# Performance work log

Measured on AMD Instinct MI355X. Metric: run time of the kernel, lower is better.

Reference implementation:

```python
import jax, jax.numpy as jnp
import numpy as np

EPS_GN = 1e-8
EPS_ATTN = 1e-8


def setup_inputs() -> dict:
    key = jax.random.key(0)
    ks = jax.random.split(key, 13)
    B, C, N = 4, 512, 2048
    s = 0.02
    return {
        "x": jax.random.normal(ks[0], (B, C, N), jnp.float32),
        "dw_w": jax.random.normal(ks[1], (C, 3), jnp.float32) * s,
        "pw_w": jax.random.normal(ks[2], (C, C), jnp.float32) * s,
        "u_w": jax.random.normal(ks[3], (2 * C, C), jnp.float32) * s,
        "u_b": jax.random.normal(ks[4], (2 * C,), jnp.float32) * s,
        "v_w": jax.random.normal(ks[5], (2 * C, C), jnp.float32) * s,
        "v_b": jax.random.normal(ks[6], (2 * C,), jnp.float32) * s,
        "h_w": jax.random.normal(ks[7], (C, C), jnp.float32) * s,
        "h_b": jax.random.normal(ks[8], (C,), jnp.float32) * s,
        "q_w": jax.random.normal(ks[9], (C, C), jnp.float32) * s,
        "k_w": jax.random.normal(ks[10], (C, C), jnp.float32) * s,
        "o_w": jax.random.normal(ks[11], (C, 2 * C), jnp.float32) * s,
        "o_b": jax.random.normal(ks[12], (C,), jnp.float32) * s,
    }


def reference(x, dw_w, pw_w, u_w, u_b, v_w, v_b, h_w, h_b, q_w, k_w, o_w, o_b):
    # x: [B, C, N]
    C = x.shape[1]
    # GroupNorm(1, C): normalize over (C, N) per sample; affine is identity-init
    # in torch but we follow the module math with default weight=1, bias=0
    mean = jnp.mean(x, axis=(1, 2), keepdims=True)
    var = jnp.var(x, axis=(1, 2), keepdims=True)
    z = (x - mean) * jax.lax.rsqrt(var + EPS_GN)

    # local depthwise conv k=3, pad=1 (cross-correlation), no bias
    zp = jnp.pad(z, ((0, 0), (0, 0), (1, 1)))
    dw = (dw_w[:, 0, None] * zp[:, :, :-2]
          + dw_w[:, 1, None] * zp[:, :, 1:-1]
          + dw_w[:, 2, None] * zp[:, :, 2:])
    # pointwise conv (no bias)
    z = z + jnp.einsum('oc,bcn->bon', pw_w, dw)

    u = jax.nn.sigmoid(jnp.einsum('oc,bcn->bon', u_w, z) + u_b[:, None])  # [B,2C,N]
    v = jnp.einsum('oc,bcn->bon', v_w, z) + v_b[:, None]                  # [B,2C,N]
    h = jnp.einsum('oc,bcn->bno', h_w, z) + h_b                           # [B,N,C]

    q = h @ q_w.T  # [B,N,C]
    k = h @ k_w.T  # [B,N,C]
    scale = 1.0 / jnp.sqrt(jnp.float32(C))

    logits = jnp.einsum('bnc,bmc->bnm', q, k) * scale
    a = jax.nn.relu(logits)
    a = a * a
    a = a / (jnp.sum(a, axis=-1, keepdims=True) + EPS_ATTN)

    av = jnp.einsum('bnm,bom->bon', a, v)  # [B,2C,N]
    y = jnp.einsum('oc,bcn->bon', o_w, u * av) + o_b[:, None]
    return x + y
```

## Files before the change

kernel.cpp:

```cpp
#include <hip/hip_runtime.h>
#include <hip/hip_bf16.h>
#include <cstdint>

typedef __bf16 bhalf;
typedef __bf16 bhalf8 __attribute__((ext_vector_type(8)));
typedef float f32x4 __attribute__((ext_vector_type(4)));

enum { EPI_Z2=0, EPI_UV=1, EPI_BIAS=2, EPI_QK=3, EPI_ATTN=4, EPI_PV=5, EPI_Y=6, EPI_ST=7 };

__device__ __forceinline__ void gl_lds16(const bhalf* g, bhalf* l) {
  __builtin_amdgcn_global_load_lds(
      (const __attribute__((address_space(1))) unsigned int*)g,
      (__attribute__((address_space(3))) unsigned int*)l,
      16, 0, 0);
}
__device__ __forceinline__ void barrier_raw() { asm volatile("s_barrier" ::: "memory"); }
#define VMW(n)  asm volatile("s_waitcnt vmcnt(" #n ")" ::: "memory")
#define LGKM0() asm volatile("s_waitcnt lgkmcnt(0)" ::: "memory")


template<int EPI>
__global__ void __launch_bounds__(512, 2)
gA(const bhalf* __restrict__ A, const bhalf* __restrict__ Bw,
   void* __restrict__ Out, void* __restrict__ Out2,
   const float* __restrict__ bias, const float* __restrict__ bias2,
   int N, int K, long sA, long sB, long sO, long sAuxf, float scale)
{
  constexpr int KSL = 256*64;
  constexpr int REG = 2*KSL;
  constexpr int DBUF = 2*REG;
  __shared__ __align__(16) char lds[2*DBUF];

  const int gx = gridDim.x, gy = gridDim.y;
  const int nwg = gx*gy;
  const int flat = blockIdx.y*gx + blockIdx.x;
  const int q8 = nwg>>3, r8 = nwg&7, xcd = flat&7, o8 = flat>>3;
  const int wsw = (xcd<r8 ? xcd*(q8+1) : r8*(q8+1)+(xcd-r8)*q8) + o8;
  const int bx = wsw % gx, by = wsw / gx;
  const int m0 = by*256, n0 = bx*256;
  const int bz = blockIdx.z;

  const bhalf* Ab = A + (long)bz*sA;
  const bhalf* Bb = Bw + (long)bz*sB;

  const int tid = threadIdx.x, wid = tid>>6, lane = tid&63;
  const int lm = lane&15, kq = lane>>4;
  const int wm = wid>>2, wn = wid&3;
  const int srow = lane>>2;
  const int csw = ((lane&3) ^ ((lane>>3)&3)) * 8;
  const int kqs = kq ^ ((lm>>1)&3);

  f32x4 acc[8][4];
  #pragma unroll
  for (int i=0;i<8;i++)
    #pragma unroll
    for (int j=0;j<4;j++) acc[i][j] = f32x4{0.f,0.f,0.f,0.f};

  auto stageA = [&](int kt){
    char* base = lds + (kt&1)*DBUF;
    const int k0 = kt*64;
    #pragma unroll
    for (int h=0; h<2; h++)
      #pragma unroll
      for (int ksl=0; ksl<2; ksl++){
        bhalf* d = (bhalf*)(base + ksl*KSL + (h*128 + wid*16)*64);
        gl_lds16(Ab + (long)(m0 + h*128 + wid*16 + srow)*K + k0 + ksl*32 + csw, d);
      }
  };
  auto stageB = [&](int kt){
    char* base = lds + (kt&1)*DBUF + REG;
    const int k0 = kt*64;
    #pragma unroll
    for (int h=0; h<2; h++)
      #pragma unroll
      for (int ksl=0; ksl<2; ksl++){
        bhalf* d = (bhalf*)(base + ksl*KSL + (h*128 + wid*16)*64);
        gl_lds16(Bb + (long)(n0 + h*128 + wid*16 + srow)*K + k0 + ksl*32 + csw, d);
      }
  };

  bhalf8 af[4][2], bf[4][2];
  auto readA = [&](int kt, int ih){
    char* base = lds + (kt&1)*DBUF;
    #pragma unroll
    for (int i2=0;i2<4;i2++)
      #pragma unroll
      for (int ksl=0;ksl<2;ksl++)
        af[i2][ksl] = *(const bhalf8*)(base + ksl*KSL + (wm*128 + ih*64 + i2*16 + lm)*64 + kqs*16);
  };
  auto readB = [&](int kt, int jh){
    char* base = lds + (kt&1)*DBUF + REG;
    #pragma unroll
    for (int j2=0;j2<2;j2++)
      #pragma unroll
      for (int ksl=0;ksl<2;ksl++)
        bf[jh*2+j2][ksl] = *(const bhalf8*)(base + ksl*KSL + (wn*64 + jh*32 + j2*16 + lm)*64 + kqs*16);
  };
  auto mfma16 = [&](int ih, int jh){
    __builtin_amdgcn_s_setprio(1);
    #pragma unroll
    for (int i2=0;i2<4;i2++)
      #pragma unroll
      for (int j2=0;j2<2;j2++)
        #pragma unroll
        for (int ksl=0;ksl<2;ksl++)
          acc[ih*4+i2][jh*2+j2] = __builtin_amdgcn_mfma_f32_16x16x32_bf16(
              af[i2][ksl], bf[jh*2+j2][ksl], acc[ih*4+i2][jh*2+j2], 0,0,0);
    __builtin_amdgcn_s_setprio(0);
  };

  const int NT = K>>6;
  stageA(0); stageB(0); stageA(1);
  for (int kt=0; kt<NT; ++kt){
    if (kt==NT-1) { VMW(0); } else { VMW(4); }
    barrier_raw();
    readA(kt,0); readB(kt,0);
    if (kt+1<NT) stageB(kt+1);
    mfma16(0,0);
    barrier_raw();
    readB(kt,1);
    mfma16(0,1);
    barrier_raw();
    readA(kt,1);
    mfma16(1,0);
    barrier_raw();
    if (kt+2<NT) stageA(kt+2);
    mfma16(1,1);
  }
  barrier_raw();

  if constexpr (EPI==EPI_ATTN){
    float rs[8][4];
    #pragma unroll
    for (int i=0;i<8;i++)
      #pragma unroll
      for (int r=0;r<4;r++) rs[i][r]=0.f;
    #pragma unroll
    for (int i=0;i<8;i++){
      #pragma unroll
      for (int j=0;j<4;j++){
        const int lcol = wn*64 + j*16 + lm;
        #pragma unroll
        for (int r=0;r<4;r++){
          const int lrow = wm*128 + i*16 + kq*4 + r;
          float v = acc[i][j][r];
          v *= scale; v = fmaxf(v,0.f); v = v*v;
          rs[i][r] += v;
          const int cb = lcol*2;
          const int lb = lrow*512 + (((cb>>5) ^ ((lrow>>2)&3))<<5) + (cb&31);
          *(bhalf*)(lds + lb) = (bhalf)v;
        }
      }
    }
    float* rd = (float*)Out2;
    #pragma unroll
    for (int i=0;i<8;i++){
      const int rbase = m0 + wm*128 + i*16 + kq*4;
      #pragma unroll
      for (int r=0;r<4;r++){
        float s = rs[i][r];
        s += __shfl_xor(s,1); s += __shfl_xor(s,2);
        s += __shfl_xor(s,4); s += __shfl_xor(s,8);
        if (lm==0) atomicAdd(rd + (long)bz*sAuxf + rbase + r, s);
      }
    }
    LGKM0();
    barrier_raw();
    char* obase = (char*)Out + 2*((long)bz*sO + (long)m0*N + n0);
    const int ldb = N*2;
    #pragma unroll
    for (int it=0; it<16; ++it){
      const int g = (it*512 + tid)*16;
      const int row = g >> 9, off = g & 511;
      const int lb = row*512 + (((off>>5) ^ ((row>>2)&3))<<5) + (off&31);
      uint4 val = *(const uint4*)(lds + lb);
      *(uint4*)(obase + (long)row*ldb + off) = val;
    }
  }
  if constexpr (EPI==EPI_UV){
    const bool uh = n0 < 1024;
    const float* bv = uh ? bias : bias2;
    const int bc0 = uh ? n0 : n0-1024;
    #pragma unroll
    for (int i=0;i<8;i++){
      #pragma unroll
      for (int j=0;j<4;j++){
        const int lcol = wn*64 + j*16 + lm;
        #pragma unroll
        for (int r=0;r<4;r++){
          const int lrow = wm*128 + i*16 + kq*4 + r;
          float v = acc[i][j][r] + bv[bc0 + lcol];
          if (uh){
            v = 1.f/(1.f + __expf(-v));
            const int cb = lcol*2;
            const int lb = lrow*512 + (((cb>>5) ^ ((lrow>>2)&3))<<5) + (cb&31);
            *(bhalf*)(lds + lb) = (bhalf)v;
          } else {
            const int lb = lcol*512 + 2*(lrow ^ ((lcol&15)<<2));
            *(bhalf*)(lds + lb) = (bhalf)v;
          }
        }
      }
    }
    LGKM0();
    barrier_raw();
    if (uh){
      char* obase = (char*)Out + 2*((long)m0*1024 + n0);
      #pragma unroll
      for (int it=0; it<16; ++it){
        const int g = (it*512 + tid)*16;
        const int row = g >> 9, off = g & 511;
        const int lb = row*512 + (((off>>5) ^ ((row>>2)&3))<<5) + (off&31);
        uint4 val = *(const uint4*)(lds + lb);
        *(uint4*)(obase + (long)row*2048 + off) = val;
      }
    } else {
      char* vb = (char*)Out2 + 2*((long)(m0>>11)*1024*2048 + (long)(n0-1024)*2048 + (m0 & 2047));
      #pragma unroll
      for (int it=0; it<16; ++it){
        const int g = (it*512 + tid)*16;
        const int row = g >> 9, off = g & 511;
        const int t0 = off >> 1;
        const int s = (row&15)<<2;
        unsigned long long lo = *(const unsigned long long*)(lds + row*512 + 2*(t0^s));
        unsigned long long hi = *(const unsigned long long*)(lds + row*512 + 2*((t0+4)^s));
        char* dst = vb + (long)row*4096 + off;
        ((unsigned long long*)dst)[0] = lo;
        ((unsigned long long*)dst)[1] = hi;
      }
    }
  }
  (void)scale; (void)bias; (void)bias2; (void)N;
}

template<int EPI>
__global__ void __launch_bounds__(256, 2)
g4k(const bhalf* __restrict__ A, const bhalf* __restrict__ Bw,
    void* __restrict__ Out, void* __restrict__ Out2,
    const float* __restrict__ bias,
    const bhalf* __restrict__ auxb, const float* __restrict__ auxf,
    const float* __restrict__ xadd,
    int M, int N, int K, long sB, int rowshift)
{
  constexpr int KSL = 256*64;
  constexpr int DBUF = 2*KSL;
  __shared__ __align__(16) char lds[2*DBUF];

  const int gx = gridDim.x, gy = gridDim.y;
  const int nwg = gx*gy;
  const int flat = blockIdx.y*gx + blockIdx.x;
  const int q8 = nwg>>3, r8 = nwg&7, xcd = flat&7, o8 = flat>>3;
  const int w = (xcd<r8 ? xcd*(q8+1) : r8*(q8+1)+(xcd-r8)*q8) + o8;
  const int bx = w % gx, by = w / gx;
  const int m0 = by*128, n0 = bx*128;

  const bhalf* Bb = Bw + (rowshift ? (long)(m0>>rowshift)*sB : 0);

  const int tid = threadIdx.x;
  const int wid = tid>>6, lane = tid&63;
  const int lm = lane&15, kq = lane>>4;
  const int wm = wid>>1, wn = wid&1;
  const int srow = lane>>2;
  const int csw = ((lane&3) ^ ((lane>>3)&3))*8;
  const int kqs = kq ^ ((lm>>1)&3);

  f32x4 acc[4][4];
  #pragma unroll
  for (int i=0;i<4;i++)
    #pragma unroll
    for (int j=0;j<4;j++) acc[i][j] = f32x4{0.f,0.f,0.f,0.f};

  auto stage = [&](int kt){
    char* base = lds + (kt&1)*DBUF;
    const int k0 = kt*64;
    #pragma unroll
    for (int c=0;c<4;c++){
      const int r0 = c*64 + wid*16;
      #pragma unroll
      for (int ksl=0; ksl<2; ksl++){
        bhalf* d = (bhalf*)(base + ksl*KSL + r0*64);
        const bhalf* g = (r0 < 128)
          ? A  + (long)(m0 + r0 + srow)*K + k0 + ksl*32 + csw
          : Bb + (long)(n0 + r0 - 128 + srow)*K + k0 + ksl*32 + csw;
        gl_lds16(g, d);
      }
    }
  };

  bhalf8 af[4][2], bf[4][2];
  auto readA = [&](int kt){
    char* base = lds + (kt&1)*DBUF;
    #pragma unroll
    for (int i2=0;i2<4;i2++)
      #pragma unroll
      for (int ksl=0;ksl<2;ksl++)
        af[i2][ksl] = *(const bhalf8*)(base + ksl*KSL + (wm*64 + i2*16 + lm)*64 + kqs*16);
  };
  auto readB = [&](int kt, int jh){
    char* base = lds + (kt&1)*DBUF;
    #pragma unroll
    for (int j2=0;j2<2;j2++)
      #pragma unroll
      for (int ksl=0;ksl<2;ksl++)
        bf[jh*2+j2][ksl] = *(const bhalf8*)(base + ksl*KSL + (128 + wn*64 + jh*32 + j2*16 + lm)*64 + kqs*16);
  };
  auto mfma16 = [&](int jh){
    __builtin_amdgcn_s_setprio(1);
    #pragma unroll
    for (int i2=0;i2<4;i2++)
      #pragma unroll
      for (int j2=0;j2<2;j2++)
        #pragma unroll
        for (int ksl=0;ksl<2;ksl++)
          acc[i2][jh*2+j2] = __builtin_amdgcn_mfma_f32_16x16x32_bf16(
              af[i2][ksl], bf[jh*2+j2][ksl], acc[i2][jh*2+j2], 0,0,0);
    __builtin_amdgcn_s_setprio(0);
  };

  const int NT = K>>6;
  stage(0); stage(1);
  for (int kt=0; kt<NT; ++kt){
    if (kt==NT-1) { VMW(0); } else { VMW(8); }
    barrier_raw();
    readA(kt); readB(kt,0);
    mfma16(0);
    barrier_raw();
    readB(kt,1);
    if (kt+2<NT) stage(kt+2);
    mfma16(1);
  }
  barrier_raw();

  if constexpr (EPI==EPI_Y){
    #pragma unroll
    for (int i=0;i<4;i++){
      #pragma unroll
      for (int j=0;j<4;j++){
        const int lcol = wn*64 + j*16 + lm;
        #pragma unroll
        for (int r=0;r<4;r++){
          const int lrow = wm*64 + i*16 + kq*4 + r;
          float v = acc[i][j][r] + bias[n0 + lcol];
          const int lb = lcol*512 + 4*(lrow ^ ((lcol&15)<<2));
          *(float*)(lds + lb) = v;
        }
      }
    }
    LGKM0();
    barrier_raw();
    const int b = m0 >> 11, nb = m0 & 2047;
    float* ob = (float*)Out + ((long)b*512 + n0)*2048 + nb;
    const float* xb = xadd + ((long)b*512 + n0)*2048 + nb;
    #pragma unroll
    for (int it=0; it<16; ++it){
      const int g = (it*256 + tid)*16;
      const int row = g >> 9, off = g & 511;
      const int t0 = off >> 2;
      const int s = (row&15)<<2;
      f32x4 vv = *(const f32x4*)(lds + row*512 + 4*(t0^s));
      f32x4 xx = *(const f32x4*)(xb + (long)row*2048 + t0);
      *(f32x4*)(ob + (long)row*2048 + t0) = vv + xx;
    }
  } else {
    char* obase; int ldb;
    if constexpr (EPI==EPI_QK){
      bool qh = n0 < 512;
      obase = (char*)(qh?Out:Out2) + 2*((long)m0*512 + (n0 - (qh?0:512)));
      ldb = 1024;
    } else {
      obase = (char*)Out + 2*((long)m0*N + n0);
      ldb = N*2;
    }
    #pragma unroll
    for (int i=0;i<4;i++){
      #pragma unroll
      for (int j=0;j<4;j++){
        const int lcol = wn*64 + j*16 + lm;
        #pragma unroll
        for (int r=0;r<4;r++){
          const int lrow = wm*64 + i*16 + kq*4 + r;
          float v = acc[i][j][r];
          if constexpr (EPI==EPI_Z2)
            v += (float)auxb[(long)(m0+lrow)*N + n0 + lcol];
          if constexpr (EPI==EPI_BIAS)
            v += bias[n0 + lcol];
          if constexpr (EPI==EPI_QK)
            v += bias[n0 + lcol];
          if constexpr (EPI==EPI_PV){
            const int rowg = m0 + lrow;
            float den = auxf[rowg];
            v *= __builtin_amdgcn_rcpf(den + 1e-8f);
            v *= (float)auxb[(long)rowg*1024 + n0 + lcol];
          }
          const int cb = lcol*2;
          const int lb = lrow*256 + (((cb>>5) ^ ((lrow>>2)&3))<<5) + (cb&31);
          *(bhalf*)(lds + lb) = (bhalf)v;
        }
      }
    }
    LGKM0();
    barrier_raw();
    #pragma unroll
    for (int it=0; it<8; ++it){
      const int g = (it*256 + tid)*16;
      const int row = g >> 8, off = g & 255;
      const int lb = row*256 + (((off>>5) ^ ((row>>2)&3))<<5) + (off&31);
      uint4 val = *(const uint4*)(lds + lb);
      *(uint4*)(obase + (long)row*ldb + off) = val;
    }
  }
  (void)M; (void)xadd; (void)bias; (void)auxb; (void)auxf;
}

struct CvtArgs { const float* src[7]; bhalf* dst[7]; int n[7]; };
__global__ void cvt_multi(CvtArgs a) {
  int seg = blockIdx.y;
  int i = (blockIdx.x*256 + threadIdx.x)*4;
  if (i >= a.n[seg]) return;
  float4 f = *(const float4*)(a.src[seg] + i);
  bhalf* d = a.dst[seg] + i;
  d[0]=(bhalf)f.x; d[1]=(bhalf)f.y; d[2]=(bhalf)f.z; d[3]=(bhalf)f.w;
}

__global__ void transpose_bf16(const bhalf* __restrict__ in, bhalf* __restrict__ out,
                               int R, int C) {
  __shared__ bhalf t[32][33];
  int r0 = blockIdx.x*32, c0 = blockIdx.y*32;
  int tx = threadIdx.x, ty = threadIdx.y;
  #pragma unroll
  for (int r=0;r<4;r++)
    t[ty + r*8][tx] = in[(long)(r0 + ty + r*8)*C + c0 + tx];
  __syncthreads();
  #pragma unroll
  for (int r=0;r<4;r++)
    out[(long)(c0 + ty + r*8)*R + r0 + tx] = t[tx][ty + r*8];
}

__global__ void qk_bias(const bhalf* __restrict__ wqk, const float* __restrict__ hb,
                        float* __restrict__ bq){
  int row = blockIdx.x*4 + (threadIdx.x>>6);
  int lane = threadIdx.x & 63;
  const bhalf* p = wqk + (long)row*512;
  float s = 0.f;
  #pragma unroll
  for (int j=0;j<8;j++) s += (float)p[lane*8+j] * hb[lane*8+j];
  for (int off=32; off; off>>=1) s += __shfl_xor(s, off);
  if (lane==0) bq[row] = s;
}

__global__ void gn_part(const float* __restrict__ x, float* __restrict__ ps, float* __restrict__ pss) {
  int b = blockIdx.y;
  const float* xb = x + (long)b*(512*2048);
  float s=0.f, ss=0.f;
  #pragma unroll
  for (int it=0; it<8; it++){
    int idx = ((it*128 + blockIdx.x)*256 + threadIdx.x)*4;
    float4 f = *(const float4*)(xb + idx);
    s  += f.x+f.y+f.z+f.w;
    ss += f.x*f.x+f.y*f.y+f.z*f.z+f.w*f.w;
  }
  for (int off=32; off; off>>=1){ s += __shfl_xor(s,off); ss += __shfl_xor(ss,off); }
  __shared__ float ls[4], lss[4];
  int wid = threadIdx.x>>6, lane = threadIdx.x&63;
  if (lane==0){ ls[wid]=s; lss[wid]=ss; }
  __syncthreads();
  if (threadIdx.x==0){
    s = ls[0]+ls[1]+ls[2]+ls[3]; ss = lss[0]+lss[1]+lss[2]+lss[3];
    ps[b*128 + blockIdx.x] = s; pss[b*128 + blockIdx.x] = ss;
  }
}

__global__ void gn_final(const float* __restrict__ ps, const float* __restrict__ pss,
                         float* __restrict__ stats) {
  int b = blockIdx.x;
  float s = ps[b*128 + threadIdx.x], ss = pss[b*128 + threadIdx.x];
  for (int off=32; off; off>>=1){ s += __shfl_xor(s,off); ss += __shfl_xor(ss,off); }
  __shared__ float l0[2], l1[2];
  int wid = threadIdx.x>>6, lane = threadIdx.x&63;
  if (lane==0){ l0[wid]=s; l1[wid]=ss; }
  __syncthreads();
  if (threadIdx.x==0){
    s = l0[0]+l0[1]; ss = l1[0]+l1[1];
    float mean = s*(1.f/1048576.f);
    float var  = ss*(1.f/1048576.f) - mean*mean;
    stats[b*2] = mean; stats[b*2+1] = rsqrtf(var + 1e-8f);
  }
}

__global__ void norm_dw_T(const float* __restrict__ x, const float* __restrict__ stats,
                          const float* __restrict__ dw_w,
                          bhalf* __restrict__ zT, bhalf* __restrict__ dwT) {
  int b = blockIdx.z, n0 = blockIdx.x*32, c0 = blockIdx.y*32;
  float mean = stats[b*2], rstd = stats[b*2+1];
  __shared__ float zs[32][35];
  int tx = threadIdx.x, ty = threadIdx.y;
  #pragma unroll
  for (int r=0;r<4;r++){
    int c = c0 + ty + r*8;
    for (int cc=tx; cc<34; cc+=32){
      int n = n0 - 1 + cc;
      float v = 0.f;
      if (n>=0 && n<2048) v = (x[((long)b*512 + c)*2048 + n] - mean)*rstd;
      zs[ty + r*8][cc] = v;
    }
  }
  __syncthreads();
  float w0 = dw_w[(c0+tx)*3+0], w1 = dw_w[(c0+tx)*3+1], w2 = dw_w[(c0+tx)*3+2];
  #pragma unroll
  for (int r=0;r<4;r++){
    int ln = ty + r*8;
    float z = zs[tx][ln+1];
    float d = w0*zs[tx][ln] + w1*zs[tx][ln+1] + w2*zs[tx][ln+2];
    long o = ((long)b*2048 + n0 + ln)*512 + c0 + tx;
    zT[o] = (bhalf)z; dwT[o] = (bhalf)d;
  }
}

extern "C" void kernel_launch(void* const* d_in, const int* in_sizes, int n_in,
                              void* d_out, int out_size, void* d_ws, size_t ws_size,
                              hipStream_t stream) {
  (void)in_sizes; (void)n_in; (void)out_size; (void)ws_size;
  const float* x    = (const float*)d_in[0];
  const float* dw_w = (const float*)d_in[1];
  const float* pw_w = (const float*)d_in[2];
  const float* u_w  = (const float*)d_in[3];
  const float* u_b  = (const float*)d_in[4];
  const float* v_w  = (const float*)d_in[5];
  const float* v_b  = (const float*)d_in[6];
  const float* h_w  = (const float*)d_in[7];
  const float* h_b  = (const float*)d_in[8];
  const float* q_w  = (const float*)d_in[9];
  const float* k_w  = (const float*)d_in[10];
  const float* o_w  = (const float*)d_in[11];
  const float* o_b  = (const float*)d_in[12];
  float* out = (float*)d_out;

  char* ws = (char*)d_ws;
  size_t off = 0;
  auto alloc = [&](size_t bytes) -> void* {
    void* p = ws + off; off = (off + bytes + 255) & ~(size_t)255; return p;
  };

  float* ps    = (float*)alloc(4*128*4);
  float* pss   = (float*)alloc(4*128*4);
  float* stats = (float*)alloc(4*2*4);
  float* rden  = (float*)alloc(4*2048*4);
  float* bq    = (float*)alloc(1024*4);
  bhalf* wb_pw = (bhalf*)alloc(512*512*2);
  bhalf* wb_uv = (bhalf*)alloc((size_t)2048*512*2);
  bhalf* wb_h  = (bhalf*)alloc(512*512*2);
  bhalf* hwT   = (bhalf*)alloc(512*512*2);
  bhalf* wb_qk = (bhalf*)alloc((size_t)1024*512*2);
  bhalf* wqk2  = (bhalf*)alloc((size_t)1024*512*2);
  bhalf* wb_o  = (bhalf*)alloc((size_t)512*1024*2);
  const size_t ACT = (size_t)4*2048*512;
  bhalf* zT   = (bhalf*)alloc(ACT*2);
  bhalf* dwT  = (bhalf*)alloc(ACT*2);
  bhalf* z2T  = (bhalf*)alloc(ACT*2);
  bhalf* ub   = (bhalf*)alloc(ACT*2*2);
  bhalf* v_fm = (bhalf*)alloc(ACT*2*2);
  bhalf* wsc  = (bhalf*)alloc((size_t)4*2048*2048*2);
  bhalf* uav  = (bhalf*)alloc(ACT*2*2);
  bhalf* qb = zT;  bhalf* kb = dwT;

  hipMemsetAsync(rden, 0, 4*2048*4, stream);

  CvtArgs ca;
  ca.src[0]=pw_w; ca.dst[0]=wb_pw;           ca.n[0]=512*512;
  ca.src[1]=u_w;  ca.dst[1]=wb_uv;           ca.n[1]=1024*512;
  ca.src[2]=v_w;  ca.dst[2]=wb_uv+1024*512;  ca.n[2]=1024*512;
  ca.src[3]=h_w;  ca.dst[3]=wb_h;            ca.n[3]=512*512;
  ca.src[4]=q_w;  ca.dst[4]=wb_qk;           ca.n[4]=512*512;
  ca.src[5]=k_w;  ca.dst[5]=wb_qk+512*512;   ca.n[5]=512*512;
  ca.src[6]=o_w;  ca.dst[6]=wb_o;            ca.n[6]=512*1024;
  cvt_multi<<<dim3(512,7), 256, 0, stream>>>(ca);

  transpose_bf16<<<dim3(16,16), dim3(32,8), 0, stream>>>(wb_h, hwT, 512, 512);
  g4k<EPI_ST><<<dim3(4,8,1), 256, 0, stream>>>(wb_qk, hwT, wqk2, nullptr,
      nullptr, nullptr, nullptr, nullptr, 1024, 512, 512, 0, 0);
  qk_bias<<<dim3(256), 256, 0, stream>>>(wb_qk, h_b, bq);

  gn_part<<<dim3(128,4), 256, 0, stream>>>(x, ps, pss);
  gn_final<<<dim3(4), 128, 0, stream>>>(ps, pss, stats);

  norm_dw_T<<<dim3(64,16,4), dim3(32,8), 0, stream>>>(x, stats, dw_w, zT, dwT);

  const float iscl = 0.044194173824159216f;
  g4k<EPI_Z2><<<dim3(4,64,1), 256, 0, stream>>>(dwT, wb_pw, z2T, nullptr,
      nullptr, zT, nullptr, nullptr, 8192, 512, 512, 0, 0);
  gA<EPI_UV><<<dim3(8,32,1), 512, 0, stream>>>(z2T, wb_uv, ub, v_fm,
      u_b, v_b, 2048, 512, 0, 0, 0, 0, 0.f);
  g4k<EPI_QK><<<dim3(8,64,1), 256, 0, stream>>>(z2T, wqk2, qb, kb,
      bq, nullptr, nullptr, nullptr, 8192, 1024, 512, 0, 0);
  gA<EPI_ATTN><<<dim3(8,8,4), 512, 0, stream>>>(qb, kb, wsc, rden,
      nullptr, nullptr, 2048, 512,
      (long)2048*512, (long)2048*512, (long)2048*2048, 2048, iscl);
  g4k<EPI_PV><<<dim3(8,64,1), 256, 0, stream>>>(wsc, v_fm, uav, nullptr,
      nullptr, ub, rden, nullptr, 8192, 1024, 2048, (long)1024*2048, 11);
  g4k<EPI_Y><<<dim3(4,64,1), 256, 0, stream>>>(uav, wb_o, out, nullptr,
      o_b, nullptr, nullptr, x, 8192, 512, 1024, 0, 0);
}
```

Measured before the change: 185.7 us.

## Store attention weights and V in FP8 and run PV GEMM with FP8 MFMA

The attention epilogue and the V half of the UV epilogue now write FP8 (e4m3) bytes instead of bf16, with new LDS swizzles sized for byte elements. A dedicated g4k8 kernel runs the PV GEMM (K=2048) with 16x16x32 fp8 MFMA and a 4-deep global-to-LDS pipeline, then applies the row-denominator normalisation and u gating in its epilogue. This halves the bytes of the largest intermediate (the 4x2048x2048 weight matrix) and doubles MFMA throughput per instruction. The cost is lower precision: unnormalised squared-ReLU weights in FP8 may saturate or lose accuracy.

```diff
diff --git a/kernel.cpp b/kernel.cpp
--- a/kernel.cpp
+++ b/kernel.cpp
@@ -8,7 +8,7 @@
 
 enum { EPI_Z2=0, EPI_UV=1, EPI_BIAS=2, EPI_QK=3, EPI_ATTN=4, EPI_PV=5, EPI_Y=6, EPI_ST=7 };
 
-__device__ __forceinline__ void gl_lds16(const bhalf* g, bhalf* l) {
+__device__ __forceinline__ void gl_lds16(const void* g, void* l) {
   __builtin_amdgcn_global_load_lds(
       (const __attribute__((address_space(1))) unsigned int*)g,
       (__attribute__((address_space(3))) unsigned int*)l,
@@ -17,6 +17,10 @@
 __device__ __forceinline__ void barrier_raw() { asm volatile("s_barrier" ::: "memory"); }
 #define VMW(n)  asm volatile("s_waitcnt vmcnt(" #n ")" ::: "memory")
 #define LGKM0() asm volatile("s_waitcnt lgkmcnt(0)" ::: "memory")
+
+__device__ __forceinline__ unsigned char to_fp8(float v){
+  return (unsigned char)(__builtin_amdgcn_cvt_pk_fp8_f32(v, v, 0, false) & 0xff);
+}
 
 
 template<int EPI>
@@ -146,9 +150,8 @@
           float v = acc[i][j][r];
           v *= scale; v = fmaxf(v,0.f); v = v*v;
           rs[i][r] += v;
-          const int cb = lcol*2;
-          const int lb = lrow*512 + (((cb>>5) ^ ((lrow>>2)&3))<<5) + (cb&31);
-          *(bhalf*)(lds + lb) = (bhalf)v;
+          const int lb = lrow*256 + ((((lcol>>4) ^ (lrow&15)))<<4) + (lcol&15);
+          *(unsigned char*)(lds + lb) = to_fp8(v);
         }
       }
     }
@@ -166,15 +169,14 @@
     }
     LGKM0();
     barrier_raw();
-    char* obase = (char*)Out + 2*((long)bz*sO + (long)m0*N + n0);
-    const int ldb = N*2;
-    #pragma unroll
-    for (int it=0; it<16; ++it){
+    char* obase = (char*)Out + (long)bz*sO + (long)m0*N + n0;
+    #pragma unroll
+    for (int it=0; it<8; ++it){
       const int g = (it*512 + tid)*16;
-      const int row = g >> 9, off = g & 511;
-      const int lb = row*512 + (((off>>5) ^ ((row>>2)&3))<<5) + (off&31);
+      const int row = g >> 8, off = g & 255;
+      const int lb = row*256 + ((((off>>4) ^ (row&15)))<<4);
       uint4 val = *(const uint4*)(lds + lb);
-      *(uint4*)(obase + (long)row*ldb + off) = val;
+      *(uint4*)(obase + (long)row*N + off) = val;
     }
   }
   if constexpr (EPI==EPI_UV){
@@ -196,8 +198,8 @@
             const int lb = lrow*512 + (((cb>>5) ^ ((lrow>>2)&3))<<5) + (cb&31);
             *(bhalf*)(lds + lb) = (bhalf)v;
           } else {
-            const int lb = lcol*512 + 2*(lrow ^ ((lcol&15)<<2));
-            *(bhalf*)(lds + lb) = (bhalf)v;
+            const int lb = lcol*256 + ((((lrow>>4) ^ (lcol&15)))<<4) + (lrow&15);
+            *(unsigned char*)(lds + lb) = to_fp8(v);
           }
         }
       }
@@ -215,36 +217,28 @@
         *(uint4*)(obase + (long)row*2048 + off) = val;
       }
     } else {
-      char* vb = (char*)Out2 + 2*((long)(m0>>11)*1024*2048 + (long)(n0-1024)*2048 + (m0 & 2047));
-      #pragma unroll
-      for (int it=0; it<16; ++it){
+      char* vb = (char*)Out2 + ((long)(m0>>11)*1024*2048 + (long)(n0-1024)*2048 + (m0 & 2047));
+      #pragma unroll
+      for (int it=0; it<8; ++it){
         const int g = (it*512 + tid)*16;
-        const int row = g >> 9, off = g & 511;
-        const int t0 = off >> 1;
-        const int s = (row&15)<<2;
-        unsigned long long lo = *(const unsigned long long*)(lds + row*512 + 2*(t0^s));
-        unsigned long long hi = *(const unsigned long long*)(lds + row*512 + 2*((t0+4)^s));
-        char* dst = vb + (long)row*4096 + off;
-        ((unsigned long long*)dst)[0] = lo;
-        ((unsigned long long*)dst)[1] = hi;
+        const int row = g >> 8, off = g & 255;
+        const int lb = row*256 + ((((off>>4) ^ (row&15)))<<4);
+        uint4 val = *(const uint4*)(lds + lb);
+        *(uint4*)(vb + (long)row*2048 + off) = val;
       }
     }
   }
   (void)scale; (void)bias; (void)bias2; (void)N;
 }
 
-template<int EPI>
 __global__ void __launch_bounds__(256, 2)
-g4k(const bhalf* __restrict__ A, const bhalf* __restrict__ Bw,
-    void* __restrict__ Out, void* __restrict__ Out2,
-    const float* __restrict__ bias,
-    const bhalf* __restrict__ auxb, const float* __restrict__ auxf,
-    const float* __restrict__ xadd,
-    int M, int N, int K, long sB, int rowshift)
+g4k8(const unsigned char* __restrict__ A, const unsigned char* __restrict__ Bw,
+     bhalf* __restrict__ Out,
+     const bhalf* __restrict__ ub, const float* __restrict__ rden,
+     int K, long sB, int rowshift)
 {
-  constexpr int KSL = 256*64;
-  constexpr int DBUF = 2*KSL;
-  __shared__ __align__(16) char lds[2*DBUF];
+  constexpr int DBUF = 256*64;
+  __shared__ __align__(16) char lds[4*DBUF];
 
   const int gx = gridDim.x, gy = gridDim.y;
   const int nwg = gx*gy;
@@ -254,7 +248,136 @@
   const int bx = w % gx, by = w / gx;
   const int m0 = by*128, n0 = bx*128;
 
-  const bhalf* Bb = Bw + (rowshift ? (long)(m0>>rowshift)*sB : 0);
+  const unsigned char* Bb = Bw + (long)(m0>>rowshift)*sB;
+
+  const int tid = threadIdx.x;
+  const int wid = tid>>6, lane = tid&63;
+  const int lm = lane&15, kq = lane>>4;
+  const int wm = wid>>1, wn = wid&1;
+  const int srow = lane>>2;
+  const int csw8 = ((lane&3) ^ ((lane>>3)&3))*16;
+  int coff[2];
+  #pragma unroll
+  for (int ksl=0; ksl<2; ksl++)
+    coff[ksl] = ((((ksl*2 + (kq>>1)) ^ ((lm>>1)&3)))<<4) + ((kq&1)<<3);
+
+  f32x4 acc[4][4];
+  #pragma unroll
+  for (int i=0;i<4;i++)
+    #pragma unroll
+    for (int j=0;j<4;j++) acc[i][j] = f32x4{0.f,0.f,0.f,0.f};
+
+  auto stage = [&](int kt){
+    char* base = lds + (kt&3)*DBUF;
+    const int k0 = kt*64;
+    #pragma unroll
+    for (int c=0;c<4;c++){
+      const int r0 = c*64 + wid*16;
+      char* d = base + r0*64;
+      const unsigned char* g = (r0 < 128)
+        ? A  + (long)(m0 + r0 + srow)*K + k0 + csw8
+        : Bb + (long)(n0 + r0 - 128 + srow)*K + k0 + csw8;
+      gl_lds16(g, d);
+    }
+  };
+
+  long af[4][2], bf[4][2];
+  auto readA = [&](int kt){
+    char* base = lds + (kt&3)*DBUF;
+    #pragma unroll
+    for (int i2=0;i2<4;i2++)
+      #pragma unroll
+      for (int ksl=0;ksl<2;ksl++)
+        af[i2][ksl] = *(const long*)(base + (wm*64 + i2*16 + lm)*64 + coff[ksl]);
+  };
+  auto readB = [&](int kt, int jh){
+    char* base = lds + (kt&3)*DBUF;
+    #pragma unroll
+    for (int j2=0;j2<2;j2++)
+      #pragma unroll
+      for (int ksl=0;ksl<2;ksl++)
+        bf[jh*2+j2][ksl] = *(const long*)(base + (128 + wn*64 + jh*32 + j2*16 + lm)*64 + coff[ksl]);
+  };
+  auto mfma16 = [&](int jh){
+    __builtin_amdgcn_s_setprio(1);
+    #pragma unroll
+    for (int i2=0;i2<4;i2++)
+      #pragma unroll
+      for (int j2=0;j2<2;j2++)
+        #pragma unroll
+        for (int ksl=0;ksl<2;ksl++)
+          acc[i2][jh*2+j2] = __builtin_amdgcn_mfma_f32_16x16x32_fp8_fp8(
+              af[i2][ksl], bf[jh*2+j2][ksl], acc[i2][jh*2+j2], 0,0,0);
+    __builtin_amdgcn_s_setprio(0);
+  };
+
+  const int NT = K>>6;
+  stage(0); stage(1); stage(2);
+  for (int kt=0; kt<NT; ++kt){
+    if (kt==NT-1)      { VMW(0); }
+    else if (kt==NT-2) { VMW(4); }
+    else               { VMW(8); }
+    barrier_raw();
+    readA(kt); readB(kt,0);
+    if (kt+3<NT) stage(kt+3);
+    mfma16(0);
+    readB(kt,1);
+    mfma16(1);
+  }
+  barrier_raw();
+
+  char* obase = (char*)Out + 2*((long)m0*1024 + n0);
+  #pragma unroll
+  for (int i=0;i<4;i++){
+    #pragma unroll
+    for (int j=0;j<4;j++){
+      const int lcol = wn*64 + j*16 + lm;
+      #pragma unroll
+      for (int r=0;r<4;r++){
+        const int lrow = wm*64 + i*16 + kq*4 + r;
+        const int rowg = m0 + lrow;
+        float v = acc[i][j][r];
+        float den = rden[rowg];
+        v *= __builtin_amdgcn_rcpf(den + 1e-8f);
+        v *= (float)ub[(long)rowg*1024 + n0 + lcol];
+        const int cb = lcol*2;
+        const int lb = lrow*256 + (((cb>>5) ^ ((lrow>>2)&3))<<5) + (cb&31);
+        *(bhalf*)(lds + lb) = (bhalf)v;
+      }
+    }
+  }
+  LGKM0();
+  barrier_raw();
+  #pragma unroll
+  for (int it=0; it<8; ++it){
+    const int g = (it*256 + tid)*16;
+    const int row = g >> 8, off = g & 255;
+    const int lb = row*256 + (((off>>5) ^ ((row>>2)&3))<<5) + (off&31);
+    uint4 val = *(const uint4*)(lds + lb);
+    *(uint4*)(obase + (long)row*2048 + off) = val;
+  }
+}
+
+template<int EPI>
+__global__ void __launch_bounds__(256, 2)
+g4k(const bhalf* __restrict__ A, const bhalf* __restrict__ Bw,
+    void* __restrict__ Out, void* __restrict__ Out2,
+    const float* __restrict__ bias,
+    const bhalf* __restrict__ auxb,
+    const float* __restrict__ xadd,
+    int M, int N, int K)
+{
+  constexpr int KSL = 256*64;
+  constexpr int DBUF = 2*KSL;
+  __shared__ __align__(16) char lds[2*DBUF];
+
+  const int gx = gridDim.x, gy = gridDim.y;
+  const int nwg = gx*gy;
+  const int flat = blockIdx.y*gx + blockIdx.x;
+  const int q8 = nwg>>3, r8 = nwg&7, xcd = flat&7, o8 = flat>>3;
+  const int w = (xcd<r8 ? xcd*(q8+1) : r8*(q8+1)+(xcd-r8)*q8) + o8;
+  const int bx = w % gx, by = w / gx;
+  const int m0 = by*128, n0 = bx*128;
 
   const int tid = threadIdx.x;
   const int wid = tid>>6, lane = tid&63;
@@ -281,7 +404,7 @@
         bhalf* d = (bhalf*)(base + ksl*KSL + r0*64);
         const bhalf* g = (r0 < 128)
           ? A  + (long)(m0 + r0 + srow)*K + k0 + ksl*32 + csw
-          : Bb + (long)(n0 + r0 - 128 + srow)*K + k0 + ksl*32 + csw;
+          : Bw + (long)(n0 + r0 - 128 + srow)*K + k0 + ksl*32 + csw;
         gl_lds16(g, d);
       }
     }
@@ -386,12 +509,6 @@
             v += bias[n0 + lcol];
           if constexpr (EPI==EPI_QK)
             v += bias[n0 + lcol];
-          if constexpr (EPI==EPI_PV){
-            const int rowg = m0 + lrow;
-            float den = auxf[rowg];
-            v *= __builtin_amdgcn_rcpf(den + 1e-8f);
-            v *= (float)auxb[(long)rowg*1024 + n0 + lcol];
-          }
           const int cb = lcol*2;
           const int lb = lrow*256 + (((cb>>5) ^ ((lrow>>2)&3))<<5) + (cb&31);
           *(bhalf*)(lds + lb) = (bhalf)v;
@@ -409,7 +526,7 @@
       *(uint4*)(obase + (long)row*ldb + off) = val;
     }
   }
-  (void)M; (void)xadd; (void)bias; (void)auxb; (void)auxf;
+  (void)M; (void)xadd; (void)bias; (void)auxb;
 }
 
 struct CvtArgs { const float* src[7]; bhalf* dst[7]; int n[7]; };
@@ -558,8 +675,8 @@
   bhalf* dwT  = (bhalf*)alloc(ACT*2);
   bhalf* z2T  = (bhalf*)alloc(ACT*2);
   bhalf* ub   = (bhalf*)alloc(ACT*2*2);
-  bhalf* v_fm = (bhalf*)alloc(ACT*2*2);
-  bhalf* wsc  = (bhalf*)alloc((size_t)4*2048*2048*2);
+  unsigned char* v_fm = (unsigned char*)alloc((size_t)4*1024*2048);
+  unsigned char* wsc  = (unsigned char*)alloc((size_t)4*2048*2048);
   bhalf* uav  = (bhalf*)alloc(ACT*2*2);
   bhalf* qb = zT;  bhalf* kb = dwT;
 
@@ -577,7 +694,7 @@
 
   transpose_bf16<<<dim3(16,16), dim3(32,8), 0, stream>>>(wb_h, hwT, 512, 512);
   g4k<EPI_ST><<<dim3(4,8,1), 256, 0, stream>>>(wb_qk, hwT, wqk2, nullptr,
-      nullptr, nullptr, nullptr, nullptr, 1024, 512, 512, 0, 0);
+      nullptr, nullptr, nullptr, 1024, 512, 512);
   qk_bias<<<dim3(256), 256, 0, stream>>>(wb_qk, h_b, bq);
 
   gn_part<<<dim3(128,4), 256, 0, stream>>>(x, ps, pss);
@@ -587,16 +704,16 @@
 
   const float iscl = 0.044194173824159216f;
   g4k<EPI_Z2><<<dim3(4,64,1), 256, 0, stream>>>(dwT, wb_pw, z2T, nullptr,
-      nullptr, zT, nullptr, nullptr, 8192, 512, 512, 0, 0);
+      nullptr, zT, nullptr, 8192, 512, 512);
   gA<EPI_UV><<<dim3(8,32,1), 512, 0, stream>>>(z2T, wb_uv, ub, v_fm,
       u_b, v_b, 2048, 512, 0, 0, 0, 0, 0.f);
   g4k<EPI_QK><<<dim3(8,64,1), 256, 0, stream>>>(z2T, wqk2, qb, kb,
-      bq, nullptr, nullptr, nullptr, 8192, 1024, 512, 0, 0);
+      bq, nullptr, nullptr, 8192, 1024, 512);
   gA<EPI_ATTN><<<dim3(8,8,4), 512, 0, stream>>>(qb, kb, wsc, rden,
       nullptr, nullptr, 2048, 512,
       (long)2048*512, (long)2048*512, (long)2048*2048, 2048, iscl);
-  g4k<EPI_PV><<<dim3(8,64,1), 256, 0, stream>>>(wsc, v_fm, uav, nullptr,
-      nullptr, ub, rden, nullptr, 8192, 1024, 2048, (long)1024*2048, 11);
+  g4k8<<<dim3(8,64,1), 256, 0, stream>>>(wsc, v_fm, uav, ub, rden,
+      2048, (long)1024*2048, 11);
   g4k<EPI_Y><<<dim3(4,64,1), 256, 0, stream>>>(uav, wb_o, out, nullptr,
-      o_b, nullptr, nullptr, x, 8192, 512, 1024, 0, 0);
-}
+      o_b, nullptr, x, 8192, 512, 1024);
+}
```

After: 178.0 us. 4.1% less time.
